# Kernel optimization log

Hardware: AMD Instinct MI355X
Metric: run time of the kernel (lower is better)

The kernel has to match this reference:

```python
import jax, jax.numpy as jnp
import numpy as np

N_QUBITS = 4
N_LAYERS = 2


def _apply_1q(state, gate, wire):
    # state: [B,2,2,2,2] complex; gate: [2,2] or [B,2,2] complex
    ax = wire + 1
    st = jnp.moveaxis(state, ax, 1)  # [B,2,...]
    if gate.ndim == 2:
        st = jnp.einsum('ij,bj...->bi...', gate, st)
    else:
        st = jnp.einsum('bij,bj...->bi...', gate, st)
    return jnp.moveaxis(st, 1, ax)


def _cnot(state, control, target):
    ca, ta = control + 1, target + 1
    s0 = jnp.take(state, 0, axis=ca)
    s1 = jnp.take(state, 1, axis=ca)
    ta2 = ta - 1 if ta > ca else ta  # axis shift after take
    s1 = jnp.flip(s1, axis=ta2)      # flip target when control=1
    return jnp.stack([s0, s1], axis=ca)


def _rx(theta):  # theta: [B] -> [B,2,2]
    c = jnp.cos(theta / 2).astype(jnp.complex64)
    s = jnp.sin(theta / 2).astype(jnp.complex64)
    return jnp.stack([jnp.stack([c, -1j * s], -1),
                      jnp.stack([-1j * s, c], -1)], -2)


def _ry(theta):  # scalar -> [2,2]
    c = jnp.cos(theta / 2).astype(jnp.complex64)
    s = jnp.sin(theta / 2).astype(jnp.complex64)
    return jnp.stack([jnp.stack([c, -s]), jnp.stack([s, c])])


def _rz(theta):  # scalar -> [2,2] diag(e^{-i t/2}, e^{i t/2})
    half = (theta / 2).astype(jnp.complex64)
    z = jnp.zeros((), jnp.complex64)
    return jnp.stack([jnp.stack([jnp.exp(-1j * half), z]),
                      jnp.stack([z, jnp.exp(1j * half)])])


def _circuit(angles, wq):
    # angles: [B,4] float32; wq: [2,4,3] float32 -> [B,4] expval PauliZ
    B = angles.shape[0]
    state = jnp.zeros((B, 2, 2, 2, 2), jnp.complex64)
    state = state.at[:, 0, 0, 0, 0].set(1.0)
    for i in range(N_QUBITS):
        state = _apply_1q(state, _rx(angles[:, i]), i)
    for layer in range(N_LAYERS):
        for i in range(N_QUBITS):
            state = _apply_1q(state, _rz(wq[layer, i, 0]), i)
            state = _apply_1q(state, _ry(wq[layer, i, 1]), i)
            state = _apply_1q(state, _rz(wq[layer, i, 2]), i)
        for i in range(N_QUBITS - 1):
            state = _cnot(state, i, i + 1)
    probs = state.real ** 2 + state.imag ** 2  # [B,2,2,2,2]
    zs = []
    for i in range(N_QUBITS):
        axes = tuple(a for a in range(1, 5) if a != i + 1)
        marg = jnp.sum(probs, axis=axes)  # [B,2]
        zs.append(marg[:, 0] - marg[:, 1])
    return jnp.stack(zs, axis=-1)  # [B,4]


def setup_inputs() -> dict:
    key = jax.random.key(0)
    ks = jax.random.split(key, 8)
    B, F = 262144, 64
    x = jax.random.normal(ks[0], (B, F), jnp.float32)
    Wp = jax.random.normal(ks[1], (N_QUBITS, F), jnp.float32) * (1.0 / np.sqrt(F))
    bp = jnp.zeros((N_QUBITS,), jnp.float32)
    wq = 0.01 * jax.random.normal(ks[2], (N_LAYERS, N_QUBITS, 3), jnp.float32)
    W1 = jax.random.normal(ks[3], (64, N_QUBITS), jnp.float32) * 0.5
    b1 = jnp.zeros((64,), jnp.float32)
    W2 = jax.random.normal(ks[4], (1, 64), jnp.float32) * 0.125
    b2 = jnp.zeros((1,), jnp.float32)
    return {"x": x, "Wp": Wp, "bp": bp, "wq": wq, "W1": W1, "b1": b1, "W2": W2, "b2": b2}


def reference(x, Wp, bp, wq, W1, b1, W2, b2):
    angles = x @ Wp.T + bp               # feature_projector -> [B,4]
    q_out = _circuit(angles, wq)         # [B,4]
    h = jax.nn.relu(q_out @ W1.T + b1)   # [B,64]
    return h @ W2.T + b2                 # [B,1]
```

## Files before the change

kernel.cpp:

```cpp
#include <hip/hip_runtime.h>

#define CB_FLOATS 1292
#define CB_V4 (CB_FLOATS / 4)


__device__ inline void gate_rz(float* ar, float* ai, int q, float th) {
    float c, s;
    __sincosf(0.5f * th, &s, &c);
    int st = 8 >> q;
    #pragma unroll
    for (int k = 0; k < 16; k++) {
        float r = ar[k], im = ai[k];
        if (k & st) {
            ar[k] = r * c - im * s;
            ai[k] = im * c + r * s;
        } else {
            ar[k] = r * c + im * s;
            ai[k] = im * c - r * s;
        }
    }
}

__device__ inline void gate_ry(float* ar, float* ai, int q, float th) {
    float c, s;
    __sincosf(0.5f * th, &s, &c);
    int st = 8 >> q;
    #pragma unroll
    for (int k = 0; k < 16; k++) {
        if (!(k & st)) {
            int k1 = k | st;
            float r0 = ar[k], i0 = ai[k], r1 = ar[k1], i1 = ai[k1];
            ar[k]  = c * r0 - s * r1;  ai[k]  = c * i0 - s * i1;
            ar[k1] = s * r0 + c * r1;  ai[k1] = s * i0 + c * i1;
        }
    }
}

__device__ inline void gate_cnot(float* ar, float* ai, int c, int t) {
    int stc = 8 >> c, stt = 8 >> t;
    #pragma unroll
    for (int k = 0; k < 16; k++) {
        if ((k & stc) && !(k & stt)) {
            int k1 = k | stt;
            float r = ar[k], im = ai[k];
            ar[k] = ar[k1]; ai[k] = ai[k1];
            ar[k1] = r;     ai[k1] = im;
        }
    }
}

__global__ void precompute_kernel(const float* __restrict__ Wp,
                                  const float* __restrict__ bp,
                                  const float* __restrict__ wq,
                                  const float* __restrict__ W1,
                                  const float* __restrict__ b1,
                                  const float* __restrict__ W2,
                                  const float* __restrict__ b2,
                                  float* __restrict__ ws) {
    int t = threadIdx.x;

    if (t < 16) {
        float ar[16], ai[16];
        #pragma unroll
        for (int k = 0; k < 16; k++) { ar[k] = 0.f; ai[k] = 0.f; }
        ar[t] = 1.f;

        for (int layer = 0; layer < 2; layer++) {
            for (int q = 0; q < 4; q++) {
                const float* w = &wq[(layer * 4 + q) * 3];
                gate_rz(ar, ai, q, w[0]);
                gate_ry(ar, ai, q, w[1]);
                gate_rz(ar, ai, q, w[2]);
            }
            for (int c = 0; c < 3; c++) gate_cnot(ar, ai, c, c + 1);
        }

        int pc = __popc(t) & 3;
        #pragma unroll
        for (int j = 0; j < 16; j++) {
            float re = ar[j], im = ai[j], vr, vi;
            switch (pc) {
                case 0: vr = re;  vi = im;  break;
                case 1: vr = im;  vi = -re; break;
                case 2: vr = -re; vi = -im; break;
                case 3: vr = -im; vi = re;  break;
            }
            ws[j * 16 + t]       = vr;
            ws[256 + j * 16 + t] = vi;
        }
    }

    for (int q = 0; q < 4; q++) ws[512 + t * 4 + q] = Wp[q * 64 + t];
    if (t < 4) ws[768 + t] = bp[t];
    if (t < 4) ws[772 + t] = 0.f;

    ws[776 + t * 8 + 0] = W1[t * 4 + 0];
    ws[776 + t * 8 + 1] = W1[t * 4 + 1];
    ws[776 + t * 8 + 2] = W1[t * 4 + 2];
    ws[776 + t * 8 + 3] = W1[t * 4 + 3];
    ws[776 + t * 8 + 4] = b1[t];
    ws[776 + t * 8 + 5] = W2[t];
    ws[776 + t * 8 + 6] = 0.f;
    ws[776 + t * 8 + 7] = 0.f;
    if (t == 0) { ws[1288] = b2[0]; ws[1289] = 0.f; ws[1290] = 0.f; ws[1291] = 0.f; }
}


__global__ __launch_bounds__(256, 4) void qmain_kernel(const float* __restrict__ x,
                                                       const float* __restrict__ cb,
                                                       float* __restrict__ out,
                                                       int B) {
    __shared__ __align__(16) float w[CB_FLOATS];
    const int t = threadIdx.x;
    {
        float4* dst = reinterpret_cast<float4*>(w);
        const float4* src = reinterpret_cast<const float4*>(cb);
        for (int i = t; i < CB_V4; i += 256) dst[i] = src[i];
    }
    __syncthreads();

    const int row = blockIdx.x * 256 + t;
    if (row >= B) return;

    const float4* __restrict__ xr = reinterpret_cast<const float4*>(x + (size_t)row * 64);

    float ang0 = w[768], ang1 = w[769], ang2 = w[770], ang3 = w[771];
    #pragma unroll 4
    for (int i = 0; i < 16; i++) {
        float4 v = xr[i];
        const float4* wt = reinterpret_cast<const float4*>(&w[512 + i * 16]);
        float4 w0 = wt[0], w1 = wt[1], w2 = wt[2], w3 = wt[3];
        ang0 = fmaf(v.x, w0.x, fmaf(v.y, w1.x, fmaf(v.z, w2.x, fmaf(v.w, w3.x, ang0))));
        ang1 = fmaf(v.x, w0.y, fmaf(v.y, w1.y, fmaf(v.z, w2.y, fmaf(v.w, w3.y, ang1))));
        ang2 = fmaf(v.x, w0.z, fmaf(v.y, w1.z, fmaf(v.z, w2.z, fmaf(v.w, w3.z, ang2))));
        ang3 = fmaf(v.x, w0.w, fmaf(v.y, w1.w, fmaf(v.z, w2.w, fmaf(v.w, w3.w, ang3))));
    }

    float c0, s0, c1, s1, c2, s2, c3, s3;
    __sincosf(0.5f * ang0, &s0, &c0);
    __sincosf(0.5f * ang1, &s1, &c1);
    __sincosf(0.5f * ang2, &s2, &c2);
    __sincosf(0.5f * ang3, &s3, &c3);
    float pre[4]  = { c0 * c1, c0 * s1, s0 * c1, s0 * s1 };
    float post[4] = { c2 * c3, c2 * s3, s2 * c3, s2 * s3 };
    float m[16];
    #pragma unroll
    for (int k = 0; k < 16; k++) m[k] = pre[k >> 2] * post[k & 3];

    float z0 = 0.f, z1 = 0.f, z2 = 0.f, z3 = 0.f;
    #pragma unroll
    for (int j = 0; j < 16; j++) {
        const float4* vr = reinterpret_cast<const float4*>(&w[j * 16]);
        const float4* vi = reinterpret_cast<const float4*>(&w[256 + j * 16]);
        float re = 0.f, im = 0.f;
        #pragma unroll
        for (int k4 = 0; k4 < 4; k4++) {
            float4 a = vr[k4];
            float4 b = vi[k4];
            re = fmaf(a.x, m[4 * k4 + 0], re);
            re = fmaf(a.y, m[4 * k4 + 1], re);
            re = fmaf(a.z, m[4 * k4 + 2], re);
            re = fmaf(a.w, m[4 * k4 + 3], re);
            im = fmaf(b.x, m[4 * k4 + 0], im);
            im = fmaf(b.y, m[4 * k4 + 1], im);
            im = fmaf(b.z, m[4 * k4 + 2], im);
            im = fmaf(b.w, m[4 * k4 + 3], im);
        }
        float p = re * re + im * im;
        z0 += (j & 8) ? -p : p;
        z1 += (j & 4) ? -p : p;
        z2 += (j & 2) ? -p : p;
        z3 += (j & 1) ? -p : p;
    }

    float acc = w[1288];
    #pragma unroll
    for (int j = 0; j < 64; j++) {
        float4 a  = *reinterpret_cast<const float4*>(&w[776 + j * 8]);
        float2 bb = *reinterpret_cast<const float2*>(&w[776 + j * 8 + 4]);
        float h = fmaf(a.x, z0, fmaf(a.y, z1, fmaf(a.z, z2, fmaf(a.w, z3, bb.x))));
        h = fmaxf(h, 0.f);
        acc = fmaf(bb.y, h, acc);
    }
    out[row] = acc;
}


extern "C" void kernel_launch(void* const* d_in, const int* in_sizes, int n_in,
                              void* d_out, int out_size, void* d_ws, size_t ws_size,
                              hipStream_t stream) {
    const float* x  = (const float*)d_in[0];
    const float* Wp = (const float*)d_in[1];
    const float* bp = (const float*)d_in[2];
    const float* wq = (const float*)d_in[3];
    const float* W1 = (const float*)d_in[4];
    const float* b1 = (const float*)d_in[5];
    const float* W2 = (const float*)d_in[6];
    const float* b2 = (const float*)d_in[7];
    float* ws = (float*)d_ws;
    float* out = (float*)d_out;

    int B = in_sizes[0] / 64;

    precompute_kernel<<<1, 64, 0, stream>>>(Wp, bp, wq, W1, b1, W2, b2, ws);

    int grid = (B + 255) / 256;
    qmain_kernel<<<grid, 256, 0, stream>>>(x, ws, out, B);
}
```

Before: 123.9 us.

## Stage x rows through per-wave LDS transpose and read constants via scalar loads

Each wave now loads its 64 rows of x with coalesced float4 reads (8 lanes per row) into a padded LDS tile, then each lane reads its own row from LDS. Before, every thread streamed its own 256-byte row with strided float4 loads. The constant block is no longer copied into shared memory; it is read straight from the global pointer, so uniform addresses can become scalar loads and the block-level sync goes away. The costs are more LDS traffic, a larger shared footprint that may limit occupancy, and hand-placed waitcnt and sched barriers.

```diff
diff --git a/kernel.cpp b/kernel.cpp
--- a/kernel.cpp
+++ b/kernel.cpp
@@ -1,7 +1,6 @@
 #include <hip/hip_runtime.h>
 
 #define CB_FLOATS 1292
-#define CB_V4 (CB_FLOATS / 4)
 
 
 __device__ inline void gate_rz(float* ar, float* ai, int q, float th) {
@@ -110,30 +109,57 @@
                                                        const float* __restrict__ cb,
                                                        float* __restrict__ out,
                                                        int B) {
-    __shared__ __align__(16) float w[CB_FLOATS];
+    __shared__ float xt[4][64 * 33];
     const int t = threadIdx.x;
-    {
-        float4* dst = reinterpret_cast<float4*>(w);
-        const float4* src = reinterpret_cast<const float4*>(cb);
-        for (int i = t; i < CB_V4; i += 256) dst[i] = src[i];
-    }
-    __syncthreads();
-
-    const int row = blockIdx.x * 256 + t;
-    if (row >= B) return;
-
-    const float4* __restrict__ xr = reinterpret_cast<const float4*>(x + (size_t)row * 64);
-
-    float ang0 = w[768], ang1 = w[769], ang2 = w[770], ang3 = w[771];
-    #pragma unroll 4
-    for (int i = 0; i < 16; i++) {
-        float4 v = xr[i];
-        const float4* wt = reinterpret_cast<const float4*>(&w[512 + i * 16]);
-        float4 w0 = wt[0], w1 = wt[1], w2 = wt[2], w3 = wt[3];
-        ang0 = fmaf(v.x, w0.x, fmaf(v.y, w1.x, fmaf(v.z, w2.x, fmaf(v.w, w3.x, ang0))));
-        ang1 = fmaf(v.x, w0.y, fmaf(v.y, w1.y, fmaf(v.z, w2.y, fmaf(v.w, w3.y, ang1))));
-        ang2 = fmaf(v.x, w0.z, fmaf(v.y, w1.z, fmaf(v.z, w2.z, fmaf(v.w, w3.z, ang2))));
-        ang3 = fmaf(v.x, w0.w, fmaf(v.y, w1.w, fmaf(v.z, w2.w, fmaf(v.w, w3.w, ang3))));
+    const int wave = t >> 6, lane = t & 63;
+    float* __restrict__ myT = xt[wave];
+    const int g = lane >> 3, h4 = (lane & 7) * 4;
+
+    const long brow = (long)blockIdx.x * 256;
+    const long row = brow + t;
+
+    float ang0 = cb[768], ang1 = cb[769], ang2 = cb[770], ang3 = cb[771];
+
+    if (brow + 256 <= (long)B) {
+        const float* __restrict__ xw = x + (brow + (long)wave * 64) * 64;
+        #pragma unroll
+        for (int c = 0; c < 2; c++) {
+            #pragma unroll
+            for (int k = 0; k < 8; k++) {
+                int r = 8 * k + g;
+                float4 v = *reinterpret_cast<const float4*>(xw + r * 64 + c * 32 + h4);
+                float* d = &myT[r * 33 + h4];
+                d[0] = v.x; d[1] = v.y; d[2] = v.z; d[3] = v.w;
+            }
+            asm volatile("s_waitcnt lgkmcnt(0)" ::: "memory");
+            __builtin_amdgcn_sched_barrier(0);
+            const float* mr = &myT[lane * 33];
+            #pragma unroll
+            for (int i = 0; i < 32; i++) {
+                float xv = mr[i];
+                const float* wp = &cb[512 + (c * 32 + i) * 4];
+                ang0 = fmaf(xv, wp[0], ang0);
+                ang1 = fmaf(xv, wp[1], ang1);
+                ang2 = fmaf(xv, wp[2], ang2);
+                ang3 = fmaf(xv, wp[3], ang3);
+            }
+            if (c == 0) {
+                asm volatile("s_waitcnt lgkmcnt(0)" ::: "memory");
+                __builtin_amdgcn_sched_barrier(0);
+            }
+        }
+    } else {
+        if (row >= (long)B) return;
+        const float4* __restrict__ xr = reinterpret_cast<const float4*>(x + row * 64);
+        #pragma unroll
+        for (int i = 0; i < 16; i++) {
+            float4 v = xr[i];
+            const float* wp = &cb[512 + i * 16];
+            ang0 = fmaf(v.x, wp[0], fmaf(v.y, wp[4], fmaf(v.z, wp[8],  fmaf(v.w, wp[12], ang0))));
+            ang1 = fmaf(v.x, wp[1], fmaf(v.y, wp[5], fmaf(v.z, wp[9],  fmaf(v.w, wp[13], ang1))));
+            ang2 = fmaf(v.x, wp[2], fmaf(v.y, wp[6], fmaf(v.z, wp[10], fmaf(v.w, wp[14], ang2))));
+            ang3 = fmaf(v.x, wp[3], fmaf(v.y, wp[7], fmaf(v.z, wp[11], fmaf(v.w, wp[15], ang3))));
+        }
     }
 
     float c0, s0, c1, s1, c2, s2, c3, s3;
@@ -150,21 +176,13 @@
     float z0 = 0.f, z1 = 0.f, z2 = 0.f, z3 = 0.f;
     #pragma unroll
     for (int j = 0; j < 16; j++) {
-        const float4* vr = reinterpret_cast<const float4*>(&w[j * 16]);
-        const float4* vi = reinterpret_cast<const float4*>(&w[256 + j * 16]);
+        const float* vr = &cb[j * 16];
+        const float* vi = &cb[256 + j * 16];
         float re = 0.f, im = 0.f;
         #pragma unroll
-        for (int k4 = 0; k4 < 4; k4++) {
-            float4 a = vr[k4];
-            float4 b = vi[k4];
-            re = fmaf(a.x, m[4 * k4 + 0], re);
-            re = fmaf(a.y, m[4 * k4 + 1], re);
-            re = fmaf(a.z, m[4 * k4 + 2], re);
-            re = fmaf(a.w, m[4 * k4 + 3], re);
-            im = fmaf(b.x, m[4 * k4 + 0], im);
-            im = fmaf(b.y, m[4 * k4 + 1], im);
-            im = fmaf(b.z, m[4 * k4 + 2], im);
-            im = fmaf(b.w, m[4 * k4 + 3], im);
+        for (int k = 0; k < 16; k++) {
+            re = fmaf(vr[k], m[k], re);
+            im = fmaf(vi[k], m[k], im);
         }
         float p = re * re + im * im;
         z0 += (j & 8) ? -p : p;
@@ -173,14 +191,13 @@
         z3 += (j & 1) ? -p : p;
     }
 
-    float acc = w[1288];
+    float acc = cb[1288];
     #pragma unroll
     for (int j = 0; j < 64; j++) {
-        float4 a  = *reinterpret_cast<const float4*>(&w[776 + j * 8]);
-        float2 bb = *reinterpret_cast<const float2*>(&w[776 + j * 8 + 4]);
-        float h = fmaf(a.x, z0, fmaf(a.y, z1, fmaf(a.z, z2, fmaf(a.w, z3, bb.x))));
-        h = fmaxf(h, 0.f);
-        acc = fmaf(bb.y, h, acc);
+        const float* mp = &cb[776 + j * 8];
+        float hdd = fmaf(mp[0], z0, fmaf(mp[1], z1, fmaf(mp[2], z2, fmaf(mp[3], z3, mp[4]))));
+        hdd = fmaxf(hdd, 0.f);
+        acc = fmaf(mp[5], hdd, acc);
     }
     out[row] = acc;
 }
```

Measured after the change: 122.6 us. No clear change (-1.0%).
